# Kernel tuning notes

Hardware: AMD Instinct MI355X
Metric: run time of the kernel (lower is better)

The kernel has to match this reference:

```python
import jax, jax.numpy as jnp
import numpy as np

BATCH = 4
SEQ = 2048
HID = 1024
N_EXP = 16
SLOTS = 128
FFN = int(HID * 4 * 2 / 3)  # 2730


def setup_inputs() -> dict:
    key = jax.random.key(0)
    k1, k2, k3, k4 = jax.random.split(key, 4)
    bs = BATCH * SEQ
    x = jax.random.normal(k1, (bs, HID), dtype=jnp.float32)
    routing_logits = jax.random.normal(k2, (bs, N_EXP, SLOTS), dtype=jnp.float32)
    # expert MLP params (no bias): up proj then down proj, SiLU activation
    w_up = jax.random.normal(k3, (N_EXP, HID, FFN), dtype=jnp.float32) * (HID ** -0.5)
    w_down = jax.random.normal(k4, (N_EXP, FFN, HID), dtype=jnp.float32) * (FFN ** -0.5)
    return {"x": x, "routing_logits": routing_logits, "w_up": w_up, "w_down": w_down, "batch": BATCH}


def reference(x, routing_logits, w_up, w_down, batch):
    bs, hid = x.shape
    seq = bs // batch
    n_exp, slots = routing_logits.shape[1], routing_logits.shape[2]
    # logits viewed as (batch, seq, n_exp*slots)
    logits = routing_logits.reshape(batch, seq, n_exp * slots)
    # dispatch: softmax over the sequence dim (each slot attends over tokens)
    dispatch = jax.nn.softmax(logits, axis=1).reshape(bs, n_exp, slots)
    # combine: softmax over (expert, slot) dim per token
    combine = jax.nn.softmax(logits, axis=-1).reshape(bs, n_exp, slots)
    # x_tilda: weighted token merge into slots  [n_exp, slots, hid]
    x_tilda = jnp.einsum('bes,bh->esh', dispatch, x)
    # per-expert MLP, batched over the expert dim (grouped GEMM)
    h = jax.nn.silu(jnp.einsum('esh,ehf->esf', x_tilda, w_up))
    e_out = jnp.einsum('esf,efh->esh', h, w_down)  # [n_exp, slots, hid]
    # combine slots back to tokens
    y = jnp.einsum('bes,esh->bh', combine, e_out)
    return y
```

## Files before the change

kernel.cpp:

```cpp
#include <hip/hip_runtime.h>
#include <hip/hip_bf16.h>
#include <math.h>

#define BS   8192
#define SEQQ 2048
#define HID  1024
#define ES   2048
#define FFN  2730
#define FFNP 2752
#define NEXP 16
#define SLOT 128

typedef __attribute__((ext_vector_type(4))) float  f32x4;
typedef __attribute__((ext_vector_type(8))) short  short8;
typedef __attribute__((ext_vector_type(4))) short  short4v;

__device__ __forceinline__ short f2bf(float f) {
    union { float f; unsigned u; } v; v.f = f;
    unsigned r = v.u + 0x7fffu + ((v.u >> 16) & 1u);
    return (short)(r >> 16);
}

__device__ __forceinline__ int swz(int row, int kk) {
    return (row << 5) + ((((kk >> 3) ^ (row >> 1)) & 3) << 3) + (kk & 7);
}

#define GLD16(gp, lp)                                                   \
    __builtin_amdgcn_global_load_lds(                                   \
        (__attribute__((address_space(1))) void*)(gp),                  \
        (__attribute__((address_space(3))) void*)(lp), 16, 0, 0)

__device__ __forceinline__ int tsw(int e) { return ((e >> 3) ^ e) & 7; }

__global__ __launch_bounds__(256) void exp_stats_kernel(const float* __restrict__ L,
                                                        short* __restrict__ DT,
                                                        short* __restrict__ CB,
                                                        float* __restrict__ rowpart,
                                                        float* __restrict__ colpart)
{
    const int t0 = (blockIdx.x & 31) << 8;
    const int et = blockIdx.x >> 5;
    const int e0 = et << 6;
    const int tid = threadIdx.x;
    const int lane = tid & 63;
    const int row = tid >> 3;
    const int seg = tid & 7;

    __shared__ short T[64 * 256];
    __shared__ float CP[4][64];

    float colacc[8];
    #pragma unroll
    for (int j = 0; j < 8; ++j) colacc[j] = 0.f;

    #pragma unroll
    for (int p = 0; p < 8; ++p) {
        const int tok = p * 32 + row;
        const float* src = L + (size_t)(t0 + tok) * ES + e0 + seg * 8;
        f32x4 a = *reinterpret_cast<const f32x4*>(src);
        f32x4 b = *reinterpret_cast<const f32x4*>(src + 4);
        float ex[8];
        #pragma unroll
        for (int j = 0; j < 4; ++j) ex[j]     = __expf(a[j]);
        #pragma unroll
        for (int j = 0; j < 4; ++j) ex[4 + j] = __expf(b[j]);
        float rs = 0.f;
        #pragma unroll
        for (int j = 0; j < 8; ++j) {
            const int e = seg * 8 + j;
            T[e * 256 + (tok ^ (((seg ^ j) & 7) << 3))] = f2bf(ex[j]);
            colacc[j] += ex[j];
            rs += ex[j];
        }
        rs += __shfl_xor(rs, 1, 64);
        rs += __shfl_xor(rs, 2, 64);
        rs += __shfl_xor(rs, 4, 64);
        if (seg == 0) rowpart[(size_t)(t0 + tok) * 32 + et] = rs;
    }
    #pragma unroll
    for (int j = 0; j < 8; ++j) {
        colacc[j] += __shfl_xor(colacc[j], 8, 64);
        colacc[j] += __shfl_xor(colacc[j], 16, 64);
        colacc[j] += __shfl_xor(colacc[j], 32, 64);
    }
    if ((lane >> 3) == 0) {
        #pragma unroll
        for (int j = 0; j < 8; ++j) CP[tid >> 6][(lane & 7) * 8 + j] = colacc[j];
    }
    __syncthreads();
    if (tid < 64)
        colpart[(size_t)(t0 >> 8) * ES + e0 + tid] =
            CP[0][tid] + CP[1][tid] + CP[2][tid] + CP[3][tid];
    {
        const int e = tid >> 2, ts = tid & 3;
        const int sw = tsw(e) << 3;
        const size_t o = (size_t)(e0 + e) * BS + t0 + ts * 64;
        #pragma unroll
        for (int q = 0; q < 8; ++q) {
            short8 w = *reinterpret_cast<const short8*>(&T[e * 256 + ((ts * 64 + q * 8) ^ sw)]);
            *reinterpret_cast<short8*>(&DT[o + q * 8]) = w;
        }
    }
    {
        #pragma unroll
        for (int p = 0; p < 8; ++p) {
            const int tok = p * 32 + row;
            short8 w;
            #pragma unroll
            for (int j = 0; j < 8; ++j) {
                const int e = seg * 8 + j;
                w[j] = T[e * 256 + (tok ^ (((seg ^ j) & 7) << 3))];
            }
            *reinterpret_cast<short8*>(&CB[(size_t)(t0 + tok) * ES + e0 + seg * 8]) = w;
        }
    }
}

__global__ __launch_bounds__(256) void rrow_kernel(const float* __restrict__ rowpart,
                                                   float* __restrict__ crcp)
{
    const int t = blockIdx.x * 256 + threadIdx.x;
    const float* p = rowpart + (size_t)t * 32;
    float s = 0.f;
    #pragma unroll
    for (int j = 0; j < 8; ++j) {
        f32x4 v = *reinterpret_cast<const f32x4*>(p + 4 * j);
        s += (v[0] + v[1]) + (v[2] + v[3]);
    }
    crcp[t] = 1.f / s;
}

__global__ __launch_bounds__(256) void rcol_kernel(const float* __restrict__ colpart,
                                                   float* __restrict__ drcp)
{
    const int g = blockIdx.x * 256 + threadIdx.x;
    const int b = g >> 11, c = g & 2047;
    float s = 0.f;
    #pragma unroll
    for (int ch = 0; ch < 8; ++ch)
        s += colpart[(size_t)(b * 8 + ch) * ES + c];
    drcp[g] = 1.f / s;
}

__global__ __launch_bounds__(256) void transpose_x(const float* __restrict__ X,
                                                   short* __restrict__ XT)
{
    __shared__ short T[64][72];
    const int tid = threadIdx.x;
    const int k0 = blockIdx.x * 64;
    const int n0 = blockIdx.y * 64;
    {
        const int kk = tid >> 2;
        const int nn = (tid & 3) * 16;
        const float* src = X + (size_t)(k0 + kk) * HID + n0 + nn;
        #pragma unroll
        for (int j = 0; j < 4; ++j) {
            f32x4 v = *reinterpret_cast<const f32x4*>(src + 4 * j);
            short4v s;
            #pragma unroll
            for (int i = 0; i < 4; ++i) s[i] = f2bf(v[i]);
            *reinterpret_cast<short4v*>(&T[kk][nn + 4 * j]) = s;
        }
    }
    __syncthreads();
    {
        const int nn  = tid >> 2;
        const int kk4 = (tid & 3) * 16;
        short8 w0, w1;
        #pragma unroll
        for (int i = 0; i < 8; ++i) w0[i] = T[kk4 + i][nn];
        #pragma unroll
        for (int i = 0; i < 8; ++i) w1[i] = T[kk4 + 8 + i][nn];
        size_t o = (size_t)(n0 + nn) * BS + k0 + kk4;
        *reinterpret_cast<short8*>(&XT[o])     = w0;
        *reinterpret_cast<short8*>(&XT[o + 8]) = w1;
    }
}

__global__ __launch_bounds__(256) void reduce_xt(const float* __restrict__ P,
                                                 const float* __restrict__ drcp,
                                                 short* __restrict__ xt)
{
    const size_t i = ((size_t)blockIdx.x * 256 + threadIdx.x) * 4;
    const int c = (int)(i >> 10);
    const size_t CH = (size_t)ES * HID;
    f32x4 s0 = *reinterpret_cast<const f32x4*>(&P[i]);
    f32x4 s1 = *reinterpret_cast<const f32x4*>(&P[i + CH]);
    f32x4 s2 = *reinterpret_cast<const f32x4*>(&P[i + 2 * CH]);
    f32x4 s3 = *reinterpret_cast<const f32x4*>(&P[i + 3 * CH]);
    const float r0 = drcp[c], r1 = drcp[ES + c], r2 = drcp[2 * ES + c], r3 = drcp[3 * ES + c];
    short4v o;
    #pragma unroll
    for (int j = 0; j < 4; ++j)
        o[j] = f2bf((s0[j] * r0 + s1[j] * r1) + (s2[j] * r2 + s3[j] * r3));
    *reinterpret_cast<short4v*>(&xt[i]) = o;
}

template<int BM, int BN, int EPI, bool NBND, bool KBND, bool BT, bool CT, bool PADW,
         typename TB, typename TC>
__device__ __forceinline__
void gemm_body(const short* __restrict__ A, const TB* __restrict__ B,
               TC* __restrict__ C, int Ndim, int Kdim,
               int lda, int ldb, int ldc,
               long sA, long sB, long sC, const float* __restrict__ aux)
{
    constexpr int BK = 32;
    A += (size_t)blockIdx.z * sA;
    B += (size_t)blockIdx.z * sB;
    C += (size_t)blockIdx.z * sC;
    const int m0 = blockIdx.x * BM;
    const int n0 = blockIdx.y * BN;
    const int tid  = threadIdx.x;
    const int lane = tid & 63;
    const int wid  = tid >> 6;
    const int wm = wid >> 1, wn = wid & 1;
    constexpr int WMT = BM / 2, WNT = BN / 2, MI = WMT / 16, NI = WNT / 16;
    constexpr int PA = BM / 64;
    constexpr int PB = BN / 64;

    __shared__ __align__(16) short As0[BM * 32], As1[BM * 32];
    __shared__ __align__(16) short Bs0[BN * 32], Bs1[BN * 32];

    f32x4 acc[MI][NI];
    #pragma unroll
    for (int mi = 0; mi < MI; ++mi)
        #pragma unroll
        for (int ni = 0; ni < NI; ++ni)
            acc[mi][ni] = (f32x4){0.f, 0.f, 0.f, 0.f};

    const int bnn = tid & 63;
    const int bks = (tid >> 6) * 8;

    auto ISSUEA = [&](short* ASP, short* BSP, int kk) {
        #pragma unroll
        for (int p = 0; p < PA; ++p) {
            const int slot = p * 256 + tid;
            const int row  = slot >> 2;
            const int seg  = (slot & 3) ^ ((row >> 1) & 3);
            GLD16(&A[(size_t)(m0 + row) * lda + kk + seg * 8],
                  &ASP[(p * 256 + wid * 64) * 8]);
        }
        if constexpr (BT) {
            #pragma unroll
            for (int p = 0; p < PB; ++p) {
                const int slot = p * 256 + tid;
                const int row  = slot >> 2;
                const int seg  = (slot & 3) ^ ((row >> 1) & 3);
                GLD16(&B[(size_t)(n0 + row) * ldb + kk + seg * 8],
                      &BSP[(p * 256 + wid * 64) * 8]);
            }
        }
    };

    auto LOADB = [&](f32x4* bF, int kk) {
        const int n_ = n0 + bnn;
        const bool nok_ = (!NBND) || (n_ < Ndim);
        #pragma unroll
        for (int j = 0; j < 8; ++j) {
            int k_ = kk + bks + j;
            bool ok_ = nok_ && ((!KBND) || (k_ < Kdim));
            bF[j >> 2][j & 3] = ok_ ? (float)B[(size_t)k_ * ldb + n_] : 0.f;
        }
    };

    auto PACKB = [&](short* BSP, const f32x4* bF) {
        short8 w;
        #pragma unroll
        for (int j = 0; j < 8; ++j) w[j] = f2bf(bF[j >> 2][j & 3]);
        *reinterpret_cast<short8*>(&BSP[swz(bnn, bks)]) = w;
    };

    auto COMPUTE = [&](const short* ASP, const short* BSP) {
        const int ar = lane & 15;
        const int ac = (lane >> 4) * 8;
        short8 af[MI], bf[NI];
        #pragma unroll
        for (int mi = 0; mi < MI; ++mi)
            af[mi] = *reinterpret_cast<const short8*>(&ASP[swz(wm * WMT + mi * 16 + ar, ac)]);
        #pragma unroll
        for (int ni = 0; ni < NI; ++ni)
            bf[ni] = *reinterpret_cast<const short8*>(&BSP[swz(wn * WNT + ni * 16 + ar, ac)]);
        #pragma unroll
        for (int mi = 0; mi < MI; ++mi)
            #pragma unroll
            for (int ni = 0; ni < NI; ++ni)
                acc[mi][ni] = __builtin_amdgcn_mfma_f32_16x16x32_bf16(
                    af[mi], bf[ni], acc[mi][ni], 0, 0, 0);
    };

    const int Kloop = KBND ? ((Kdim + 31) & ~31) : Kdim;
    const int nt = Kloop / BK;

    if constexpr (BT) {
        ISSUEA(As0, Bs0, 0);
        __syncthreads();
        for (int t = 0; t < nt; t += 2) {
            ISSUEA(As1, Bs1, (t + 1) * BK);
            COMPUTE(As0, Bs0);
            __syncthreads();
            const bool p2 = (t + 2 < nt);
            if (p2) ISSUEA(As0, Bs0, (t + 2) * BK);
            COMPUTE(As1, Bs1);
            __syncthreads();
        }
    } else {
        f32x4 bFa[2], bFb[2];
        LOADB(bFa, 0);
        __builtin_amdgcn_sched_barrier(0);
        ISSUEA(As0, Bs0, 0);
        __builtin_amdgcn_sched_barrier(0);
        LOADB(bFb, BK);
        PACKB(Bs0, bFa);
        asm volatile("s_waitcnt vmcnt(8) lgkmcnt(0)" ::: "memory");
        __builtin_amdgcn_s_barrier();

        for (int t = 0; t < nt; t += 2) {
            {
                ISSUEA(As1, Bs1, (t + 1) * BK);
                __builtin_amdgcn_sched_barrier(0);
                const bool pf = (t + 2 < nt);
                if (pf) LOADB(bFa, (t + 2) * BK);
                COMPUTE(As0, Bs0);
                PACKB(Bs1, bFb);
                if (pf) asm volatile("s_waitcnt vmcnt(8) lgkmcnt(0)" ::: "memory");
                else    asm volatile("s_waitcnt vmcnt(0) lgkmcnt(0)" ::: "memory");
                __builtin_amdgcn_s_barrier();
            }
            {
                const bool p2 = (t + 2 < nt);
                const bool p3 = (t + 3 < nt);
                if (p2) ISSUEA(As0, Bs0, (t + 2) * BK);
                __builtin_amdgcn_sched_barrier(0);
                if (p3) LOADB(bFb, (t + 3) * BK);
                COMPUTE(As1, Bs1);
                if (p2) PACKB(Bs0, bFa);
                if (p3) asm volatile("s_waitcnt vmcnt(8) lgkmcnt(0)" ::: "memory");
                else    asm volatile("s_waitcnt vmcnt(0) lgkmcnt(0)" ::: "memory");
                __builtin_amdgcn_s_barrier();
            }
        }
    }

    #pragma unroll
    for (int mi = 0; mi < MI; ++mi) {
        #pragma unroll
        for (int ni = 0; ni < NI; ++ni) {
            const int n = n0 + wn * WNT + ni * 16 + (lane & 15);
            if (NBND && !PADW && n >= Ndim) continue;
            const int mbase = m0 + wm * WMT + mi * 16 + (lane >> 4) * 4;
            if constexpr (CT) {
                short4v sv;
                #pragma unroll
                for (int r = 0; r < 4; ++r) sv[r] = f2bf(acc[mi][ni][r]);
                *reinterpret_cast<short4v*>(&C[(size_t)n * ldc + mbase]) = sv;
            } else {
                #pragma unroll
                for (int r = 0; r < 4; ++r) {
                    float v = acc[mi][ni][r];
                    if (EPI == 1)      v = v / (1.f + __expf(-v));
                    else if (EPI == 2) v = v * aux[mbase + r];
                    if constexpr (sizeof(TC) == 2) C[(size_t)(mbase + r) * ldc + n] = f2bf(v);
                    else                           C[(size_t)(mbase + r) * ldc + n] = v;
                }
            }
        }
    }
}

__global__ __launch_bounds__(256) void g1_gemm(const short* A, const short* B, float* C) {
    gemm_body<128, 128, 0, false, false, true, false, false, short, float>(
        A, B, C, HID, 2048, BS, BS, HID, 2048L, 2048L, (long)ES * HID, nullptr);
}
__global__ __launch_bounds__(256) void g1f_gemm(const short* A, const float* B, float* C) {
    gemm_body<128, 64, 0, false, false, false, false, false, float, float>(
        A, B, C, HID, 2048, BS, HID, HID, 2048L, 2048L * HID, (long)ES * HID, nullptr);
}
__global__ __launch_bounds__(256) void g2_gemm(const short* A, const float* B, short* C) {
    gemm_body<128, 64, 1, true, false, false, false, true, float, short>(
        A, B, C, FFN, HID, HID, FFN, FFNP,
        (long)SLOT * HID, (long)HID * FFN, (long)SLOT * FFNP, nullptr);
}
__global__ __launch_bounds__(256) void g3_gemm(const short* A, const float* B, short* C) {
    gemm_body<64, 64, 0, false, true, false, true, false, float, short>(
        A, B, C, HID, FFN, FFNP, HID, ES,
        (long)SLOT * FFNP, (long)FFN * HID, (long)SLOT, nullptr);
}
__global__ __launch_bounds__(256) void g4_gemm(const short* A, const short* B, float* C,
                                               const float* crcp) {
    gemm_body<128, 128, 2, false, false, true, false, false, short, float>(
        A, B, C, HID, ES, ES, ES, HID, 0, 0, 0, crcp);
}


extern "C" void kernel_launch(void* const* d_in, const int* in_sizes, int n_in,
                              void* d_out, int out_size, void* d_ws, size_t ws_size,
                              hipStream_t stream)
{
    const float* x      = (const float*)d_in[0];
    const float* logits = (const float*)d_in[1];
    const float* w_up   = (const float*)d_in[2];
    const float* w_down = (const float*)d_in[3];
    float* y = (float*)d_out;

    float* wsf     = (float*)d_ws;
    float* drcp    = wsf;
    float* crcp    = wsf + 8192;
    float* rowpart = wsf + 16384;
    float* colpart = rowpart + (size_t)8192 * 32;
    short* DT      = (short*)(colpart + (size_t)32 * 2048);
    short* CB      = DT + (size_t)ES * BS;
    float* part    = (float*)(CB + (size_t)BS * ES);
    short* xt      = (short*)(part + (size_t)4 * ES * HID);
    short* h       = xt + (size_t)ES * HID;
    short* eoutT   = h + (size_t)NEXP * SLOT * FFNP;
    short* xT      = eoutT + (size_t)HID * ES;
    const size_t need_full = (size_t)((char*)(xT + (size_t)HID * BS) - (char*)d_ws);
    const bool use_bt = ws_size >= need_full;


    exp_stats_kernel<<<1024, 256, 0, stream>>>(logits, DT, CB, rowpart, colpart);
    rrow_kernel<<<32, 256, 0, stream>>>(rowpart, crcp);
    rcol_kernel<<<32, 256, 0, stream>>>(colpart, drcp);

    if (use_bt) {
        transpose_x<<<dim3(128, 16, 1), 256, 0, stream>>>(x, xT);
        g1_gemm<<<dim3(16, 8, 4), 256, 0, stream>>>(DT, xT, part);
    } else {
        g1f_gemm<<<dim3(16, 16, 4), 256, 0, stream>>>(DT, x, part);
    }

    reduce_xt<<<2048, 256, 0, stream>>>(part, drcp, xt);

    g2_gemm<<<dim3(1, 43, NEXP), 256, 0, stream>>>(xt, w_up, h);

    g3_gemm<<<dim3(2, 16, NEXP), 256, 0, stream>>>(h, w_down, eoutT);

    g4_gemm<<<dim3(64, 8, 1), 256, 0, stream>>>(CB, eoutT, y, crcp);
}
```

Before: 321.1 us.

## Vectorize fp32 B-operand loads and store split-K partials in bf16

```diff
diff --git a/kernel.cpp b/kernel.cpp
--- a/kernel.cpp
+++ b/kernel.cpp
@@ -12,6 +12,7 @@
 #define SLOT 128
 
 typedef __attribute__((ext_vector_type(4))) float  f32x4;
+typedef __attribute__((ext_vector_type(2))) float  f32x2;
 typedef __attribute__((ext_vector_type(8))) short  short8;
 typedef __attribute__((ext_vector_type(4))) short  short4v;
 
@@ -19,6 +20,12 @@
     union { float f; unsigned u; } v; v.f = f;
     unsigned r = v.u + 0x7fffu + ((v.u >> 16) & 1u);
     return (short)(r >> 16);
+}
+
+__device__ __forceinline__ float bf2f(short s) {
+    union { unsigned u; float f; } v;
+    v.u = ((unsigned)(unsigned short)s) << 16;
+    return v.f;
 }
 
 __device__ __forceinline__ int swz(int row, int kk) {
@@ -177,27 +184,28 @@
     }
 }
 
-__global__ __launch_bounds__(256) void reduce_xt(const float* __restrict__ P,
+__global__ __launch_bounds__(256) void reduce_xt(const short* __restrict__ P,
                                                  const float* __restrict__ drcp,
                                                  short* __restrict__ xt)
 {
     const size_t i = ((size_t)blockIdx.x * 256 + threadIdx.x) * 4;
     const int c = (int)(i >> 10);
     const size_t CH = (size_t)ES * HID;
-    f32x4 s0 = *reinterpret_cast<const f32x4*>(&P[i]);
-    f32x4 s1 = *reinterpret_cast<const f32x4*>(&P[i + CH]);
-    f32x4 s2 = *reinterpret_cast<const f32x4*>(&P[i + 2 * CH]);
-    f32x4 s3 = *reinterpret_cast<const f32x4*>(&P[i + 3 * CH]);
+    short4v s0 = *reinterpret_cast<const short4v*>(&P[i]);
+    short4v s1 = *reinterpret_cast<const short4v*>(&P[i + CH]);
+    short4v s2 = *reinterpret_cast<const short4v*>(&P[i + 2 * CH]);
+    short4v s3 = *reinterpret_cast<const short4v*>(&P[i + 3 * CH]);
     const float r0 = drcp[c], r1 = drcp[ES + c], r2 = drcp[2 * ES + c], r3 = drcp[3 * ES + c];
     short4v o;
     #pragma unroll
     for (int j = 0; j < 4; ++j)
-        o[j] = f2bf((s0[j] * r0 + s1[j] * r1) + (s2[j] * r2 + s3[j] * r3));
+        o[j] = f2bf((bf2f(s0[j]) * r0 + bf2f(s1[j]) * r1) +
+                    (bf2f(s2[j]) * r2 + bf2f(s3[j]) * r3));
     *reinterpret_cast<short4v*>(&xt[i]) = o;
 }
 
 template<int BM, int BN, int EPI, bool NBND, bool KBND, bool BT, bool CT, bool PADW,
-         typename TB, typename TC>
+         int FW, typename TB, typename TC>
 __device__ __forceinline__
 void gemm_body(const short* __restrict__ A, const TB* __restrict__ B,
                TC* __restrict__ C, int Ndim, int Kdim,
@@ -228,8 +236,8 @@
         for (int ni = 0; ni < NI; ++ni)
             acc[mi][ni] = (f32x4){0.f, 0.f, 0.f, 0.f};
 
-    const int bnn = tid & 63;
-    const int bks = (tid >> 6) * 8;
+    const int fn = (tid & 15) * 4;
+    const int fk = (tid >> 4) * 2;
 
     auto ISSUEA = [&](short* ASP, short* BSP, int kk) {
         #pragma unroll
@@ -253,21 +261,34 @@
     };
 
     auto LOADB = [&](f32x4* bF, int kk) {
-        const int n_ = n0 + bnn;
-        const bool nok_ = (!NBND) || (n_ < Ndim);
-        #pragma unroll
-        for (int j = 0; j < 8; ++j) {
-            int k_ = kk + bks + j;
-            bool ok_ = nok_ && ((!KBND) || (k_ < Kdim));
-            bF[j >> 2][j & 3] = ok_ ? (float)B[(size_t)k_ * ldb + n_] : 0.f;
+        const int n_ = n0 + fn;
+        #pragma unroll
+        for (int r = 0; r < 2; ++r) {
+            const int k_ = kk + fk + r;
+            const bool okk = (!KBND) || (k_ < Kdim);
+            if constexpr (NBND) {
+                if (okk && (n_ + 3 < Ndim)) {
+                    bF[r] = *reinterpret_cast<const f32x4*>(&B[(size_t)k_ * ldb + n_]);
+                } else {
+                    #pragma unroll
+                    for (int i = 0; i < 4; ++i)
+                        bF[r][i] = (okk && (n_ + i < Ndim))
+                                       ? B[(size_t)k_ * ldb + n_ + i] : 0.f;
+                }
+            } else {
+                bF[r] = okk ? *reinterpret_cast<const f32x4*>(&B[(size_t)k_ * ldb + n_])
+                            : (f32x4){0.f, 0.f, 0.f, 0.f};
+            }
         }
     };
 
     auto PACKB = [&](short* BSP, const f32x4* bF) {
-        short8 w;
-        #pragma unroll
-        for (int j = 0; j < 8; ++j) w[j] = f2bf(bF[j >> 2][j & 3]);
-        *reinterpret_cast<short8*>(&BSP[swz(bnn, bks)]) = w;
+        #pragma unroll
+        for (int i = 0; i < 4; ++i) {
+            unsigned lo = (unsigned short)f2bf(bF[0][i]);
+            unsigned hi = (unsigned short)f2bf(bF[1][i]);
+            *reinterpret_cast<unsigned*>(&BSP[swz(fn + i, fk)]) = lo | (hi << 16);
+        }
     };
 
     auto COMPUTE = [&](const short* ASP, const short* BSP) {
@@ -311,7 +332,7 @@
         __builtin_amdgcn_sched_barrier(0);
         LOADB(bFb, BK);
         PACKB(Bs0, bFa);
-        asm volatile("s_waitcnt vmcnt(8) lgkmcnt(0)" ::: "memory");
+        asm volatile("s_waitcnt vmcnt(2) lgkmcnt(0)" ::: "memory");
         __builtin_amdgcn_s_barrier();
 
         for (int t = 0; t < nt; t += 2) {
@@ -322,7 +343,7 @@
                 if (pf) LOADB(bFa, (t + 2) * BK);
                 COMPUTE(As0, Bs0);
                 PACKB(Bs1, bFb);
-                if (pf) asm volatile("s_waitcnt vmcnt(8) lgkmcnt(0)" ::: "memory");
+                if (pf) asm volatile("s_waitcnt vmcnt(2) lgkmcnt(0)" ::: "memory");
                 else    asm volatile("s_waitcnt vmcnt(0) lgkmcnt(0)" ::: "memory");
                 __builtin_amdgcn_s_barrier();
             }
@@ -334,7 +355,7 @@
                 if (p3) LOADB(bFb, (t + 3) * BK);
                 COMPUTE(As1, Bs1);
                 if (p2) PACKB(Bs0, bFa);
-                if (p3) asm volatile("s_waitcnt vmcnt(8) lgkmcnt(0)" ::: "memory");
+                if (p3) asm volatile("s_waitcnt vmcnt(2) lgkmcnt(0)" ::: "memory");
                 else    asm volatile("s_waitcnt vmcnt(0) lgkmcnt(0)" ::: "memory");
                 __builtin_amdgcn_s_barrier();
             }
@@ -367,27 +388,27 @@
     }
 }
 
-__global__ __launch_bounds__(256) void g1_gemm(const short* A, const short* B, float* C) {
-    gemm_body<128, 128, 0, false, false, true, false, false, short, float>(
+__global__ __launch_bounds__(256) void g1_gemm(const short* A, const short* B, short* C) {
+    gemm_body<128, 128, 0, false, false, true, false, false, 0, short, short>(
         A, B, C, HID, 2048, BS, BS, HID, 2048L, 2048L, (long)ES * HID, nullptr);
 }
-__global__ __launch_bounds__(256) void g1f_gemm(const short* A, const float* B, float* C) {
-    gemm_body<128, 64, 0, false, false, false, false, false, float, float>(
+__global__ __launch_bounds__(256) void g1f_gemm(const short* A, const float* B, short* C) {
+    gemm_body<128, 64, 0, false, false, false, false, false, 4, float, short>(
         A, B, C, HID, 2048, BS, HID, HID, 2048L, 2048L * HID, (long)ES * HID, nullptr);
 }
 __global__ __launch_bounds__(256) void g2_gemm(const short* A, const float* B, short* C) {
-    gemm_body<128, 64, 1, true, false, false, false, true, float, short>(
+    gemm_body<128, 64, 1, true, false, false, false, true, 4, float, short>(
         A, B, C, FFN, HID, HID, FFN, FFNP,
         (long)SLOT * HID, (long)HID * FFN, (long)SLOT * FFNP, nullptr);
 }
 __global__ __launch_bounds__(256) void g3_gemm(const short* A, const float* B, short* C) {
-    gemm_body<64, 64, 0, false, true, false, true, false, float, short>(
+    gemm_body<64, 64, 0, false, true, false, true, false, 4, float, short>(
         A, B, C, HID, FFN, FFNP, HID, ES,
         (long)SLOT * FFNP, (long)FFN * HID, (long)SLOT, nullptr);
 }
 __global__ __launch_bounds__(256) void g4_gemm(const short* A, const short* B, float* C,
                                                const float* crcp) {
-    gemm_body<128, 128, 2, false, false, true, false, false, short, float>(
+    gemm_body<128, 128, 2, false, false, true, false, false, 0, short, float>(
         A, B, C, HID, ES, ES, ES, HID, 0, 0, 0, crcp);
 }
 
@@ -409,8 +430,8 @@
     float* colpart = rowpart + (size_t)8192 * 32;
     short* DT      = (short*)(colpart + (size_t)32 * 2048);
     short* CB      = DT + (size_t)ES * BS;
-    float* part    = (float*)(CB + (size_t)BS * ES);
-    short* xt      = (short*)(part + (size_t)4 * ES * HID);
+    short* part    = CB + (size_t)BS * ES;
+    short* xt      = part + (size_t)4 * ES * HID;
     short* h       = xt + (size_t)ES * HID;
     short* eoutT   = h + (size_t)NEXP * SLOT * FFNP;
     short* xT      = eoutT + (size_t)HID * ES;
```

After: 288.3 us. -10.2%, faster.
